# Performance work log

Hardware: AMD Instinct MI355X
Metric: run time of the kernel (lower is better)

The kernel has to match this reference:

```python
import jax, jax.numpy as jnp
import numpy as np

D = 1536          # d_model
H = 12            # n_heads // 2 for chunk attention
HD = D // H       # head dim = 128
MAXC = 256        # max_chunks
MAXLEN = 1024     # max_seq_length (size embedding table)
THRESH = 0.5      # boundary threshold (init value of the learned param)


def _gelu(v):
    return jax.nn.gelu(v, approximate=False)  # torch nn.GELU default (erf)


def _cos(a, b):
    # F.cosine_similarity with eps=1e-8
    na = jnp.maximum(jnp.linalg.norm(a, axis=-1), 1e-8)
    nb = jnp.maximum(jnp.linalg.norm(b, axis=-1), 1e-8)
    return jnp.sum(a * b, axis=-1) / (na * nb)


def _interp1d(y, L_out):
    # F.interpolate(mode='linear', align_corners=False) on [B, L_in] -> [B, L_out]
    L_in = y.shape[1]
    src = jnp.clip((jnp.arange(L_out, dtype=y.dtype) + 0.5) * (L_in / L_out) - 0.5, 0.0, L_in - 1)
    i0 = jnp.floor(src).astype(jnp.int32)
    i1 = jnp.minimum(i0 + 1, L_in - 1)
    w = src - i0.astype(y.dtype)
    return y[:, i0] * (1.0 - w) + y[:, i1] * w


def setup_inputs() -> dict:
    key = jax.random.key(0)
    ks = jax.random.split(key, 16)
    B, S = 4, 1024
    rn = lambda k, sh, s=0.02: jax.random.normal(k, sh, dtype=jnp.float32) * s
    return {
        'x': jax.random.normal(ks[0], (B, S, D), dtype=jnp.float32),
        'Wp': rn(ks[1], (D, D)), 'bp': jnp.zeros((D,), jnp.float32),
        'detW1': rn(ks[2], (3, D, 2 * D)), 'detb1': jnp.zeros((3, D), jnp.float32),
        'detW2': rn(ks[3], (3, D // 2, D)), 'detb2': jnp.zeros((3, D // 2), jnp.float32),
        'detW3': rn(ks[4], (3, D // 2)), 'detb3': jnp.zeros((3,), jnp.float32),
        'in_proj_w': rn(ks[5], (3 * D, D)), 'in_proj_b': jnp.zeros((3 * D,), jnp.float32),
        'out_w': rn(ks[6], (D, D)), 'out_b': jnp.zeros((D,), jnp.float32),
        'size_emb': jax.random.normal(ks[7], (MAXLEN, D), dtype=jnp.float32),
        'pos_enc': rn(ks[8], (1, MAXC, D)),
        'procW1': rn(ks[9], (2 * D, D)), 'procb1': jnp.zeros((2 * D,), jnp.float32),
        'procW2': rn(ks[10], (D, 2 * D)), 'procb2': jnp.zeros((D,), jnp.float32),
        'ln_g': jnp.ones((D,), jnp.float32), 'ln_b': jnp.zeros((D,), jnp.float32),
    }


def reference(x, Wp, bp, detW1, detb1, detW2, detb2, detW3, detb3,
              in_proj_w, in_proj_b, out_w, out_b, size_emb, pos_enc,
              procW1, procb1, procW2, procb2, ln_g, ln_b):
    B, S, d = x.shape
    # ---- DynamicSemanticChunker ----
    x_ling = x @ Wp.T + bp
    sims = []
    for scale in (1, 2, 4):
        xs = x_ling[:, ::scale]
        cs = _cos(xs[:, :-1], xs[:, 1:])           # [B, L-1]
        sims.append(_interp1d(cs, S - 1))           # [B, S-1]
    avg_sim = jnp.mean(jnp.stack(sims, 0), axis=0)
    base = 0.5 * (1.0 - avg_sim)
    bi = jnp.concatenate([x[:, :-1], x[:, 1:]], axis=-1)  # [B, S-1, 2d]
    h1 = _gelu(jnp.einsum('bsk,ndk->nbsd', bi, detW1) + detb1[:, None, None, :])
    h2 = _gelu(jnp.einsum('nbsd,nhd->nbsh', h1, detW2) + detb2[:, None, None, :])
    learned = jax.nn.sigmoid(jnp.einsum('nbsh,nh->nbs', h2, detW3) + detb3[:, None, None])
    avg_learned = jnp.mean(learned, axis=0)
    final = 0.6 * base + 0.4 * avg_learned
    boundaries = jnp.concatenate([jnp.ones((B, 1), x.dtype), final], axis=1)  # [B, S]
    # ---- EnhancedChunkLayer.create_chunks ----
    # contiguous ragged chunks == segments between boundary positions
    seg = jnp.cumsum((boundaries > THRESH).astype(jnp.int32), axis=1) - 1      # [B, S]
    # per-chunk MHA == full-seq attention with block-diagonal same-segment mask
    qkv = x @ in_proj_w.T + in_proj_b
    q, k, v = jnp.split(qkv, 3, axis=-1)
    q = q.reshape(B, S, H, HD)
    k = k.reshape(B, S, H, HD)
    v = v.reshape(B, S, H, HD)
    scores = jnp.einsum('bqhd,bkhd->bhqk', q, k) / np.sqrt(HD).astype(np.float32)
    same = (seg[:, None, :, None] == seg[:, None, None, :])                    # [B,1,S,S]
    scores = jnp.where(same, scores, jnp.asarray(-1e9, scores.dtype))
    attn = jax.nn.softmax(scores, axis=-1)
    ctx = jnp.einsum('bhqk,bkhd->bqhd', attn, v).reshape(B, S, d)
    attn_out = ctx @ out_w.T + out_b                                           # [B, S, d]
    # masked segment mean pooling; chunks with id >= MAXC are truncated away
    onehot = (seg[..., None] == jnp.arange(MAXC)).astype(x.dtype)              # [B,S,MAXC]
    sums = jnp.einsum('bsm,bsd->bmd', onehot, attn_out)
    counts = jnp.sum(onehot, axis=1)                                            # [B,MAXC]
    mean = sums / jnp.maximum(counts, 1.0)[..., None]
    clen = jnp.minimum(counts.astype(jnp.int32), MAXLEN - 1)
    sizes = size_emb[clen]                                                      # [B,MAXC,d]
    chunk = jnp.where(counts[..., None] > 0, mean + sizes, 0.0)                 # zero-pad empty
    # ---- pos encoding + chunk_processor (Linear->GELU->Linear->LayerNorm) ----
    chunk = chunk + pos_enc
    h = _gelu(chunk @ procW1.T + procb1)
    y = h @ procW2.T + procb2
    mu = jnp.mean(y, axis=-1, keepdims=True)
    var = jnp.var(y, axis=-1, keepdims=True)
    y = (y - mu) / jnp.sqrt(var + 1e-5) * ln_g + ln_b
    return y  # [B, MAXC, d]
```

## Files before the change

kernel.cpp:

```cpp
#include <hip/hip_runtime.h>
#include <hip/hip_bf16.h>
#include <math.h>

#define D_ 1536
#define S_ 1024
#define B_ 4
#define H_ 12
#define HD_ 128
#define MAXC_ 256

typedef __bf16 bf16x8_t __attribute__((ext_vector_type(8)));
typedef float f32x4_t __attribute__((ext_vector_type(4)));

__device__ __forceinline__ float gelu_f(float v) {
    return 0.5f * v * (1.0f + erff(v / 1.41421356237f));
}

__device__ __forceinline__ void split2(float a, __hip_bfloat16& h, __hip_bfloat16& l) {
    h = __float2bfloat16(a);
    l = __float2bfloat16(a - __bfloat162float(h));
}

__device__ __forceinline__ void xcd_swizzle(int& bx, int& by, int gx, int gy) {
    int nwg = gx * gy;
    int orig = by * gx + bx;
    int xcd = orig & 7;
    int q = nwg >> 3, r = nwg & 7;
    int wg = (xcd < r ? xcd * (q + 1) : r * (q + 1) + (xcd - r) * q) + (orig >> 3);
    bx = wg % gx;
    by = wg / gx;
}

template<int BM, int SPLITA, int SPLITB, int ACT, int OUT>
__global__ __launch_bounds__(256, 2)
void mfma3_gemm(const float* __restrict__ Af, const __hip_bfloat16* __restrict__ Ah,
                const __hip_bfloat16* __restrict__ Al,
                const float* __restrict__ Bf, const __hip_bfloat16* __restrict__ Bh,
                const __hip_bfloat16* __restrict__ Bl,
                const float* __restrict__ bias, int biasStride,
                float* __restrict__ Cf, __hip_bfloat16* __restrict__ Ch, __hip_bfloat16* __restrict__ Cl,
                const float* __restrict__ w3, float* __restrict__ lg,
                int K, int lda, int ldb, int ldc,
                long long aBound, long long azS, long long bzS, long long czS)
{
    __shared__ __align__(16) __hip_bfloat16 Ash[BM * 32], Asl[BM * 32];
    __shared__ __align__(16) __hip_bfloat16 Bsh[128 * 32], Bsl[128 * 32];
    const int z = blockIdx.z;
    int bxi = blockIdx.x, byi = blockIdx.y;
    xcd_swizzle(bxi, byi, gridDim.x, gridDim.y);
    const int bm = byi * BM, bn = bxi * 128;
    const int tid = threadIdx.x, lane = tid & 63, wave = tid >> 6;
    const int wm = (BM == 128) ? (wave >> 1) : 0;
    const int wn = (BM == 128) ? (wave & 1) : wave;
    constexpr int NF = (BM == 128) ? 4 : 2;
    constexpr int WC = NF * 16;
    const int fr = lane & 15, kg = lane >> 4;
    f32x4_t acc[4][NF] = {};
    constexpr int RSH = (BM == 128) ? 1 : 2;
    constexpr int NBA = (BM == 128) ? 2 : 1;
    const int ar = tid >> RSH, akb = tid & ((1 << RSH) - 1);
    const int br = tid >> 1, bkb = tid & 1;

    bf16x8_t rAh[NBA], rAl[NBA], rBh[2], rBl[2];
    float4 rAf[NBA][2], rBf[2][2];

    auto load_tile = [&](int k0) {
        #pragma unroll
        for (int j = 0; j < NBA; ++j) {
            int skg = akb * NBA + j;
            long long base = (long long)(bm + ar) * lda + azS * z + k0 + skg * 8;
            if (SPLITA) {
                #pragma unroll
                for (int q = 0; q < 2; ++q) {
                    float4 v = make_float4(0.f, 0.f, 0.f, 0.f);
                    if (base + q * 4 + 4 <= aBound) v = *reinterpret_cast<const float4*>(&Af[base + q * 4]);
                    rAf[j][q] = v;
                }
            } else {
                rAh[j] = *reinterpret_cast<const bf16x8_t*>(&Ah[base]);
                rAl[j] = *reinterpret_cast<const bf16x8_t*>(&Al[base]);
            }
        }
        #pragma unroll
        for (int j = 0; j < 2; ++j) {
            int skg = bkb * 2 + j;
            long long base = (long long)(bn + br) * ldb + bzS * z + k0 + skg * 8;
            if (SPLITB) {
                #pragma unroll
                for (int q = 0; q < 2; ++q)
                    rBf[j][q] = *reinterpret_cast<const float4*>(&Bf[base + q * 4]);
            } else {
                rBh[j] = *reinterpret_cast<const bf16x8_t*>(&Bh[base]);
                rBl[j] = *reinterpret_cast<const bf16x8_t*>(&Bl[base]);
            }
        }
    };

    auto write_tile = [&]() {
        #pragma unroll
        for (int j = 0; j < NBA; ++j) {
            int skg = akb * NBA + j;
            int blk = ar * 4 + (skg ^ ((ar >> 1) & 3));
            if (SPLITA) {
                float av[8];
                *reinterpret_cast<float4*>(&av[0]) = rAf[j][0];
                *reinterpret_cast<float4*>(&av[4]) = rAf[j][1];
                __hip_bfloat16 hh[8], ll[8];
                #pragma unroll
                for (int q = 0; q < 8; ++q) split2(av[q], hh[q], ll[q]);
                *reinterpret_cast<bf16x8_t*>(&Ash[blk * 8]) = *reinterpret_cast<bf16x8_t*>(hh);
                *reinterpret_cast<bf16x8_t*>(&Asl[blk * 8]) = *reinterpret_cast<bf16x8_t*>(ll);
            } else {
                *reinterpret_cast<bf16x8_t*>(&Ash[blk * 8]) = rAh[j];
                *reinterpret_cast<bf16x8_t*>(&Asl[blk * 8]) = rAl[j];
            }
        }
        #pragma unroll
        for (int j = 0; j < 2; ++j) {
            int skg = bkb * 2 + j;
            int blk = br * 4 + (skg ^ ((br >> 1) & 3));
            if (SPLITB) {
                float av[8];
                *reinterpret_cast<float4*>(&av[0]) = rBf[j][0];
                *reinterpret_cast<float4*>(&av[4]) = rBf[j][1];
                __hip_bfloat16 hh[8], ll[8];
                #pragma unroll
                for (int q = 0; q < 8; ++q) split2(av[q], hh[q], ll[q]);
                *reinterpret_cast<bf16x8_t*>(&Bsh[blk * 8]) = *reinterpret_cast<bf16x8_t*>(hh);
                *reinterpret_cast<bf16x8_t*>(&Bsl[blk * 8]) = *reinterpret_cast<bf16x8_t*>(ll);
            } else {
                *reinterpret_cast<bf16x8_t*>(&Bsh[blk * 8]) = rBh[j];
                *reinterpret_cast<bf16x8_t*>(&Bsl[blk * 8]) = rBl[j];
            }
        }
    };

    load_tile(0);
    write_tile();
    __syncthreads();

    for (int k0 = 0; k0 < K; k0 += 32) {
        const bool has_next = (k0 + 32) < K;
        if (has_next) load_tile(k0 + 32);

        bf16x8_t fah[4], fal[4], fbh[NF], fbl[NF];
        #pragma unroll
        for (int m = 0; m < 4; ++m) {
            int row = wm * 64 + m * 16 + fr;
            int blk = row * 4 + (kg ^ ((row >> 1) & 3));
            fah[m] = *reinterpret_cast<const bf16x8_t*>(&Ash[blk * 8]);
            fal[m] = *reinterpret_cast<const bf16x8_t*>(&Asl[blk * 8]);
        }
        #pragma unroll
        for (int n = 0; n < NF; ++n) {
            int row = wn * WC + n * 16 + fr;
            int blk = row * 4 + (kg ^ ((row >> 1) & 3));
            fbh[n] = *reinterpret_cast<const bf16x8_t*>(&Bsh[blk * 8]);
            fbl[n] = *reinterpret_cast<const bf16x8_t*>(&Bsl[blk * 8]);
        }
        #pragma unroll
        for (int m = 0; m < 4; ++m)
            #pragma unroll
            for (int n = 0; n < NF; ++n) {
                acc[m][n] = __builtin_amdgcn_mfma_f32_16x16x32_bf16(fah[m], fbh[n], acc[m][n], 0, 0, 0);
                acc[m][n] = __builtin_amdgcn_mfma_f32_16x16x32_bf16(fah[m], fbl[n], acc[m][n], 0, 0, 0);
                acc[m][n] = __builtin_amdgcn_mfma_f32_16x16x32_bf16(fal[m], fbh[n], acc[m][n], 0, 0, 0);
            }

        if (has_next) {
            __syncthreads();
            write_tile();
            __syncthreads();
        }
    }

    const int fq = lane >> 4;
    const float* bp_ = bias + (long long)biasStride * z;

    if constexpr (OUT == 2) {
        float psum[4][4] = {};
        #pragma unroll
        for (int n = 0; n < NF; ++n) {
            int col = bn + wn * WC + n * 16 + fr;
            float bv = bp_[col];
            float wv = w3[(long long)biasStride * z + col];
            #pragma unroll
            for (int m = 0; m < 4; ++m)
                #pragma unroll
                for (int r = 0; r < 4; ++r) {
                    float v = acc[m][n][r] + bv;
                    v = gelu_f(v);
                    psum[m][r] += v * wv;
                }
        }
        #pragma unroll
        for (int m = 0; m < 4; ++m)
            #pragma unroll
            for (int r = 0; r < 4; ++r) {
                float p = psum[m][r];
                p += __shfl_xor(p, 1);
                p += __shfl_xor(p, 2);
                p += __shfl_xor(p, 4);
                p += __shfl_xor(p, 8);
                if (fr == 0) {
                    int row = bm + wm * 64 + m * 16 + fq * 4 + r;
                    atomicAdd(&lg[czS * z + row], p);
                }
            }
        return;
    }

    #pragma unroll
    for (int n = 0; n < NF; ++n) {
        int col = bn + wn * WC + n * 16 + fr;
        float bv = bp_[col];
        #pragma unroll
        for (int m = 0; m < 4; ++m) {
            int row0 = bm + wm * 64 + m * 16 + fq * 4;
            #pragma unroll
            for (int r = 0; r < 4; ++r) {
                float v = acc[m][n][r] + bv;
                if (ACT == 1) v = gelu_f(v);
                long long ci = czS * z + (long long)(row0 + r) * ldc + col;
                if constexpr (OUT == 0) {
                    Cf[ci] = v;
                } else {
                    __hip_bfloat16 hh, ll;
                    split2(v, hh, ll);
                    Ch[ci] = hh; Cl[ci] = ll;
                }
            }
        }
    }
}

template<int ACT, int OUT_BF16>
__global__ __launch_bounds__(256)
void mfma_gemm(const __hip_bfloat16* __restrict__ A, const __hip_bfloat16* __restrict__ Bw,
               const float* __restrict__ bias, void* __restrict__ Cout,
               int M, int N, int K)
{
    __shared__ __align__(16) __hip_bfloat16 As[128 * 32];
    __shared__ __align__(16) __hip_bfloat16 Bs[128 * 32];
    const int tid = threadIdx.x;
    const int lane = tid & 63;
    const int wave = tid >> 6;
    const int wm = wave >> 1, wn = wave & 1;
    int bxi = blockIdx.x, byi = blockIdx.y;
    xcd_swizzle(bxi, byi, gridDim.x, gridDim.y);
    const int bm = byi * 128, bn = bxi * 128;
    const int srow = tid >> 2;
    const int skg = tid & 3;
    const int fr = lane & 15, kg = lane >> 4;

    f32x4_t acc[4][4] = {};
    bf16x8_t rA[2], rB[2];

    auto load_tile = [&](int k0) {
        #pragma unroll
        for (int it = 0; it < 2; ++it) {
            int r = srow + it * 64;
            rA[it] = *reinterpret_cast<const bf16x8_t*>(&A[(long long)(bm + r) * K + k0 + skg * 8]);
            rB[it] = *reinterpret_cast<const bf16x8_t*>(&Bw[(long long)(bn + r) * K + k0 + skg * 8]);
        }
    };
    auto write_tile = [&]() {
        #pragma unroll
        for (int it = 0; it < 2; ++it) {
            int r = srow + it * 64;
            int blk = r * 4 + (skg ^ ((r >> 1) & 3));
            *reinterpret_cast<bf16x8_t*>(&As[blk * 8]) = rA[it];
            *reinterpret_cast<bf16x8_t*>(&Bs[blk * 8]) = rB[it];
        }
    };

    load_tile(0);
    write_tile();
    __syncthreads();

    for (int k0 = 0; k0 < K; k0 += 32) {
        const bool has_next = (k0 + 32) < K;
        if (has_next) load_tile(k0 + 32);

        bf16x8_t af[4], bfr[4];
        #pragma unroll
        for (int m = 0; m < 4; ++m) {
            int row = wm * 64 + m * 16 + fr;
            af[m] = *reinterpret_cast<const bf16x8_t*>(&As[(row * 4 + (kg ^ ((row >> 1) & 3))) * 8]);
        }
        #pragma unroll
        for (int n = 0; n < 4; ++n) {
            int row = wn * 64 + n * 16 + fr;
            bfr[n] = *reinterpret_cast<const bf16x8_t*>(&Bs[(row * 4 + (kg ^ ((row >> 1) & 3))) * 8]);
        }
        #pragma unroll
        for (int m = 0; m < 4; ++m)
            #pragma unroll
            for (int n = 0; n < 4; ++n)
                acc[m][n] = __builtin_amdgcn_mfma_f32_16x16x32_bf16(af[m], bfr[n], acc[m][n], 0, 0, 0);

        if (has_next) {
            __syncthreads();
            write_tile();
            __syncthreads();
        }
    }
    const int fq = lane >> 4;
    #pragma unroll
    for (int n = 0; n < 4; ++n) {
        int col = bn + wn * 64 + n * 16 + fr;
        float bv = bias[col];
        #pragma unroll
        for (int m = 0; m < 4; ++m) {
            int row0 = bm + wm * 64 + m * 16 + fq * 4;
            #pragma unroll
            for (int r = 0; r < 4; ++r) {
                float v = acc[m][n][r] + bv;
                if (ACT == 1) v = gelu_f(v);
                if (OUT_BF16) ((__hip_bfloat16*)Cout)[(long long)(row0 + r) * N + col] = __float2bfloat16(v);
                else          ((float*)Cout)[(long long)(row0 + r) * N + col] = v;
            }
        }
    }
}

__global__ __launch_bounds__(256)
void f2b_kernel(const float* __restrict__ in, __hip_bfloat16* __restrict__ out, int n4)
{
    int i = blockIdx.x * 256 + threadIdx.x;
    if (i >= n4) return;
    float4 v = reinterpret_cast<const float4*>(in)[i];
    __hip_bfloat16 h[4] = { __float2bfloat16(v.x), __float2bfloat16(v.y),
                            __float2bfloat16(v.z), __float2bfloat16(v.w) };
    reinterpret_cast<short4*>(out)[i] = *reinterpret_cast<short4*>(h);
}

__global__ __launch_bounds__(256)
void split_kernel(const float* __restrict__ in, __hip_bfloat16* __restrict__ oh,
                  __hip_bfloat16* __restrict__ ol, int n4)
{
    int i = blockIdx.x * 256 + threadIdx.x;
    if (i >= n4) return;
    float4 v = reinterpret_cast<const float4*>(in)[i];
    __hip_bfloat16 h[4], l[4];
    split2(v.x, h[0], l[0]); split2(v.y, h[1], l[1]);
    split2(v.z, h[2], l[2]); split2(v.w, h[3], l[3]);
    reinterpret_cast<short4*>(oh)[i] = *reinterpret_cast<short4*>(h);
    reinterpret_cast<short4*>(ol)[i] = *reinterpret_cast<short4*>(l);
}

__global__ __launch_bounds__(64)
void cs_kernel(const float* __restrict__ xl, float* __restrict__ cs)
{
    int idx = blockIdx.x;
    int b = blockIdx.y;
    int sc, i, off;
    if (idx < 1023)      { sc = 1; i = idx;        off = 0;    }
    else if (idx < 1534) { sc = 2; i = idx - 1023; off = 1023; }
    else                 { sc = 4; i = idx - 1534; off = 1534; }
    const float* ra = xl + ((long long)b * S_ + (long long)i * sc) * D_;
    const float* rb = ra + (long long)sc * D_;
    int lane = threadIdx.x;
    float dp = 0.f, na = 0.f, nb = 0.f;
    for (int d = lane; d < D_; d += 64) {
        float a = ra[d], c = rb[d];
        dp += a * c; na += a * a; nb += c * c;
    }
    #pragma unroll
    for (int o = 32; o; o >>= 1) {
        dp += __shfl_down(dp, o);
        na += __shfl_down(na, o);
        nb += __shfl_down(nb, o);
    }
    if (lane == 0) {
        float den = fmaxf(sqrtf(na), 1e-8f) * fmaxf(sqrtf(nb), 1e-8f);
        cs[(long long)b * 1789 + off + i] = dp / den;
    }
}

__global__ void final_kernel(const float* __restrict__ cs, const float* __restrict__ logits,
                             const float* __restrict__ b3, float* __restrict__ fin)
{
    int g = blockIdx.x * blockDim.x + threadIdx.x;
    if (g >= B_ * 1023) return;
    int b = g / 1023, t = g % 1023;
    const float* c = cs + (long long)b * 1789;
    float v0 = c[t];
    const float r2 = (float)(511.0 / 1023.0);
    float src2 = fminf(fmaxf(((float)t + 0.5f) * r2 - 0.5f, 0.0f), 510.0f);
    int i0 = (int)floorf(src2);
    int i1 = min(i0 + 1, 510);
    float w2 = src2 - (float)i0;
    float v1 = c[1023 + i0] * (1.0f - w2) + c[1023 + i1] * w2;
    const float r4 = (float)(255.0 / 1023.0);
    float src4 = fminf(fmaxf(((float)t + 0.5f) * r4 - 0.5f, 0.0f), 254.0f);
    int j0 = (int)floorf(src4);
    int j1 = min(j0 + 1, 254);
    float w4 = src4 - (float)j0;
    float v2 = c[1534 + j0] * (1.0f - w4) + c[1534 + j1] * w4;
    float avg = ((v0 + v1) + v2) / 3.0f;
    float base = 0.5f * (1.0f - avg);
    int rr = b * 1024 + t;
    float l0 = 1.0f / (1.0f + expf(-(logits[0 * 4096 + rr] + b3[0])));
    float l1 = 1.0f / (1.0f + expf(-(logits[1 * 4096 + rr] + b3[1])));
    float l2 = 1.0f / (1.0f + expf(-(logits[2 * 4096 + rr] + b3[2])));
    float al = ((l0 + l1) + l2) / 3.0f;
    fin[g] = 0.6f * base + 0.4f * al;
}

__global__ __launch_bounds__(64)
void seg_kernel(const float* __restrict__ fin, int* __restrict__ seg)
{
    int b = blockIdx.x;
    int lane = threadIdx.x;
    int loc[16];
    int cnt = 0;
    #pragma unroll
    for (int i = 0; i < 16; ++i) {
        int t = lane * 16 + i;
        int v = (t >= 1 && fin[b * 1023 + t - 1] > 0.5f) ? 1 : 0;
        cnt += v;
        loc[i] = cnt;
    }
    int inc = cnt;
    #pragma unroll
    for (int o = 1; o < 64; o <<= 1) {
        int u = __shfl_up(inc, o);
        if (lane >= o) inc += u;
    }
    int ex = inc - cnt;
    #pragma unroll
    for (int i = 0; i < 16; ++i) {
        int t = lane * 16 + i;
        seg[b * S_ + t] = ex + loc[i];
    }
}

__global__ void segrange_kernel(const float* __restrict__ fin, const int* __restrict__ seg,
                                int* __restrict__ sstart, int* __restrict__ send,
                                int* __restrict__ cfirst, int* __restrict__ ccount)
{
    int gs = blockIdx.x * blockDim.x + threadIdx.x;
    if (gs >= B_ * S_) return;
    int b = gs / S_, s = gs % S_;
    const float* f = fin + b * 1023;
    int t = s;
    while (t > 0 && !(f[t - 1] > 0.5f)) --t;
    int e = s;
    while (e < 1023 && !(f[e] > 0.5f)) ++e;
    sstart[gs] = t;
    send[gs] = e + 1;
    if (s == t) {
        int m = seg[gs];
        if (m < MAXC_) { cfirst[b * MAXC_ + m] = t; ccount[b * MAXC_ + m] = e + 1 - t; }
    }
}

__global__ __launch_bounds__(64)
void attn_kernel(const __hip_bfloat16* __restrict__ qkv, const int* __restrict__ sstart,
                 const int* __restrict__ send, __hip_bfloat16* __restrict__ ctx)
{
    int gs = blockIdx.x;
    int h = blockIdx.y;
    int lane = threadIdx.x;
    int b = gs >> 10;
    const __hip_bfloat16* qrow = qkv + (long long)gs * 4608 + h * HD_;
    float q0 = __bfloat162float(qrow[lane]), q1 = __bfloat162float(qrow[lane + 64]);
    int st = sstart[gs], en = send[gs];
    float m = -INFINITY, l = 0.f, a0 = 0.f, a1 = 0.f;
    for (int t = st; t < en; ++t) {
        long long krow = ((long long)(b * S_ + t)) * 4608 + 1536 + h * HD_;
        float p = q0 * __bfloat162float(qkv[krow + lane]) + q1 * __bfloat162float(qkv[krow + lane + 64]);
        #pragma unroll
        for (int o = 32; o; o >>= 1) p += __shfl_xor(p, o);
        p = p / 11.3137084989847603904f;
        float nm = fmaxf(m, p);
        float scale = expf(m - nm);
        float w = expf(p - nm);
        long long vrow = ((long long)(b * S_ + t)) * 4608 + 3072 + h * HD_;
        l = l * scale + w;
        a0 = a0 * scale + w * __bfloat162float(qkv[vrow + lane]);
        a1 = a1 * scale + w * __bfloat162float(qkv[vrow + lane + 64]);
        m = nm;
    }
    float inv = 1.0f / l;
    ctx[(long long)gs * D_ + h * HD_ + lane] = __float2bfloat16(a0 * inv);
    ctx[(long long)gs * D_ + h * HD_ + lane + 64] = __float2bfloat16(a1 * inv);
}

__global__ __launch_bounds__(256)
void chunk_kernel(const float* __restrict__ attn_out, const int* __restrict__ cfirst,
                  const int* __restrict__ ccount, const float* __restrict__ size_emb,
                  const float* __restrict__ pos_enc, __hip_bfloat16* __restrict__ chunk)
{
    int m = blockIdx.x, b = blockIdx.y;
    int cnt = ccount[b * MAXC_ + m];
    for (int d = threadIdx.x; d < D_; d += 256) {
        float v;
        if (cnt > 0) {
            int first = cfirst[b * MAXC_ + m];
            float ssum = 0.f;
            for (int t = 0; t < cnt; ++t)
                ssum += attn_out[((long long)(b * S_ + first + t)) * D_ + d];
            float mean = ssum / (float)cnt;
            int clen = min(cnt, 1023);
            v = mean + size_emb[(long long)clen * D_ + d];
        } else {
            v = 0.f;
        }
        v += pos_enc[m * D_ + d];
        chunk[((long long)(b * MAXC_ + m)) * D_ + d] = __float2bfloat16(v);
    }
}

__global__ __launch_bounds__(256)
void ln_kernel(const float* __restrict__ y0, const float* __restrict__ g,
               const float* __restrict__ bb, float* __restrict__ out)
{
    int r = blockIdx.x;
    const float* row = y0 + (long long)r * D_;
    float loc[6];
    float s = 0.f;
    #pragma unroll
    for (int i = 0; i < 6; ++i) { loc[i] = row[threadIdx.x + i * 256]; s += loc[i]; }
    __shared__ float red[256];
    red[threadIdx.x] = s; __syncthreads();
    for (int o = 128; o; o >>= 1) { if (threadIdx.x < o) red[threadIdx.x] += red[threadIdx.x + o]; __syncthreads(); }
    float mu = red[0] / 1536.0f;
    __syncthreads();
    float s2 = 0.f;
    #pragma unroll
    for (int i = 0; i < 6; ++i) { float d = loc[i] - mu; s2 += d * d; }
    red[threadIdx.x] = s2; __syncthreads();
    for (int o = 128; o; o >>= 1) { if (threadIdx.x < o) red[threadIdx.x] += red[threadIdx.x + o]; __syncthreads(); }
    float var = red[0] / 1536.0f;
    float inv = 1.0f / sqrtf(var + 1e-5f);
    #pragma unroll
    for (int i = 0; i < 6; ++i) {
        int d = threadIdx.x + i * 256;
        out[(long long)r * D_ + d] = (loc[i] - mu) * inv * g[d] + bb[d];
    }
}

extern "C" void kernel_launch(void* const* d_in, const int* in_sizes, int n_in,
                              void* d_out, int out_size, void* d_ws, size_t ws_size,
                              hipStream_t stream)
{
    const float* x         = (const float*)d_in[0];
    const float* Wp        = (const float*)d_in[1];
    const float* bp        = (const float*)d_in[2];
    const float* detW1     = (const float*)d_in[3];
    const float* detb1     = (const float*)d_in[4];
    const float* detW2     = (const float*)d_in[5];
    const float* detb2     = (const float*)d_in[6];
    const float* detW3     = (const float*)d_in[7];
    const float* detb3     = (const float*)d_in[8];
    const float* in_proj_w = (const float*)d_in[9];
    const float* in_proj_b = (const float*)d_in[10];
    const float* out_w     = (const float*)d_in[11];
    const float* out_b     = (const float*)d_in[12];
    const float* size_emb  = (const float*)d_in[13];
    const float* pos_enc   = (const float*)d_in[14];
    const float* procW1    = (const float*)d_in[15];
    const float* procb1    = (const float*)d_in[16];
    const float* procW2    = (const float*)d_in[17];
    const float* procb2    = (const float*)d_in[18];
    const float* ln_g      = (const float*)d_in[19];
    const float* ln_b      = (const float*)d_in[20];
    float* out = (float*)d_out;

    const bool big = ws_size >= (size_t)192 * 1024 * 1024;

    char* ws = (char*)d_ws;
    float*          xlingf = (float*)(ws + 0);
    __hip_bfloat16* Wph    = (__hip_bfloat16*)(ws + 25165824);
    __hip_bfloat16* Wpl    = (__hip_bfloat16*)(ws + 29884416);
    __hip_bfloat16* h1h    = (__hip_bfloat16*)(ws + 0);
    __hip_bfloat16* h1l    = (__hip_bfloat16*)(ws + 37748736);
    __hip_bfloat16* W1h_s  = (__hip_bfloat16*)(ws + 75497472);
    __hip_bfloat16* W1l_s  = (__hip_bfloat16*)(ws + 94371840);
    __hip_bfloat16* W2h_s  = (__hip_bfloat16*)(ws + 75497472);
    __hip_bfloat16* W2l_s  = (__hip_bfloat16*)(ws + 82575360);
    __hip_bfloat16* xh     = (__hip_bfloat16*)(ws + 75497472);
    __hip_bfloat16* xl     = (__hip_bfloat16*)(ws + 88082432);
    __hip_bfloat16* W1h_b  = (__hip_bfloat16*)(ws + 125829120);
    __hip_bfloat16* W1l_b  = (__hip_bfloat16*)(ws + 154140672);
    __hip_bfloat16* W2h_b  = (__hip_bfloat16*)(ws + 125829120);
    __hip_bfloat16* W2l_b  = (__hip_bfloat16*)(ws + 132907008);
    __hip_bfloat16* xb_s       = (__hip_bfloat16*)(ws + 0);
    __hip_bfloat16* in_proj_wb = (__hip_bfloat16*)(ws + 12582912);
    __hip_bfloat16* qkvb       = (__hip_bfloat16*)(ws + 26738688);
    __hip_bfloat16* ctxb       = (__hip_bfloat16*)(ws + 64487424);
    __hip_bfloat16* out_wb     = (__hip_bfloat16*)(ws + 12582912);
    float*          attno      = (float*)(ws + 77070336);
    __hip_bfloat16* chunkb     = (__hip_bfloat16*)(ws + 0);
    __hip_bfloat16* procW1b    = (__hip_bfloat16*)(ws + 3145728);
    __hip_bfloat16* hmidb      = (__hip_bfloat16*)(ws + 12582912);
    __hip_bfloat16* procW2b    = (__hip_bfloat16*)(ws + 18874368);
    float*          y0         = (float*)(ws + 28311552);
    char* sm = ws + 113246208;
    float* csb    = (float*)(sm + 0);
    float* logits = (float*)(sm + 28672);
    float* fin    = (float*)(sm + 77824);
    int*   seg    = (int*)  (sm + 94208);
    int*   sstart = (int*)  (sm + 110592);
    int*   send   = (int*)  (sm + 126976);
    int*   cfirst = (int*)  (sm + 143360);
    int*   ccount = (int*)  (sm + 147456);

    const long long SLICE_W1 = 4718592LL;
    const long long SLICE_W2 = 1179648LL;
    const long long H1_Z     = 6291456LL;

    split_kernel<<<(2359296 / 4 + 255) / 256, 256, 0, stream>>>(Wp, Wph, Wpl, 2359296 / 4);
    if (big)
        split_kernel<<<(6291456 / 4 + 255) / 256, 256, 0, stream>>>(x, xh, xl, 6291456 / 4);

    if (big)
        mfma3_gemm<128, 0, 0, 0, 0><<<dim3(12, 32, 1), 256, 0, stream>>>(
            nullptr, xh, xl, nullptr, Wph, Wpl, bp, 0,
            xlingf, nullptr, nullptr, nullptr, nullptr,
            1536, 1536, 1536, 1536, 0LL, 0LL, 0LL, 0LL);
    else
        mfma3_gemm<64, 1, 0, 0, 0><<<dim3(12, 64, 1), 256, 0, stream>>>(
            x, nullptr, nullptr, nullptr, Wph, Wpl, bp, 0,
            xlingf, nullptr, nullptr, nullptr, nullptr,
            1536, 1536, 1536, 1536, 6291456LL, 0LL, 0LL, 0LL);
    cs_kernel<<<dim3(1789, 4), 64, 0, stream>>>(xlingf, csb);

    if (big) {
        split_kernel<<<(14155776 / 4 + 255) / 256, 256, 0, stream>>>(detW1, W1h_b, W1l_b, 14155776 / 4);
        mfma3_gemm<128, 0, 0, 1, 1><<<dim3(12, 32, 3), 256, 0, stream>>>(
            nullptr, xh, xl, nullptr, W1h_b, W1l_b, detb1, 1536,
            nullptr, h1h, h1l, nullptr, nullptr,
            3072, 1536, 3072, 1536, 0LL, 0LL, SLICE_W1, H1_Z);
    } else {
        split_kernel<<<(2 * 4718592 / 4 + 255) / 256, 256, 0, stream>>>(detW1, W1h_s, W1l_s, 2 * 4718592 / 4);
        mfma3_gemm<128, 1, 0, 1, 1><<<dim3(12, 32, 2), 256, 0, stream>>>(
            x, nullptr, nullptr, nullptr, W1h_s, W1l_s, detb1, 1536,
            nullptr, h1h, h1l, nullptr, nullptr,
            3072, 1536, 3072, 1536, 6291456LL, 0LL, SLICE_W1, H1_Z);
        split_kernel<<<(4718592 / 4 + 255) / 256, 256, 0, stream>>>(detW1 + 2 * SLICE_W1, W1h_s, W1l_s, 4718592 / 4);
        mfma3_gemm<64, 1, 0, 1, 1><<<dim3(12, 64, 1), 256, 0, stream>>>(
            x, nullptr, nullptr, nullptr, W1h_s, W1l_s, detb1 + 2 * 1536, 1536,
            nullptr, h1h + 2 * H1_Z, h1l + 2 * H1_Z, nullptr, nullptr,
            3072, 1536, 3072, 1536, 6291456LL, 0LL, 0LL, 0LL);
    }

    __hip_bfloat16* W2h = big ? W2h_b : W2h_s;
    __hip_bfloat16* W2l = big ? W2l_b : W2l_s;
    split_kernel<<<(3538944 / 4 + 255) / 256, 256, 0, stream>>>(detW2, W2h, W2l, 3538944 / 4);
    hipMemsetAsync(logits, 0, 3 * 4096 * sizeof(float), stream);
    mfma3_gemm<128, 0, 0, 1, 2><<<dim3(6, 32, 3), 256, 0, stream>>>(
        nullptr, h1h, h1l, nullptr, W2h, W2l, detb2, 768,
        nullptr, nullptr, nullptr, detW3, logits,
        1536, 1536, 1536, 768, 0LL, H1_Z, SLICE_W2, 4096LL);

    final_kernel<<<16, 256, 0, stream>>>(csb, logits, detb3, fin);
    seg_kernel<<<4, 64, 0, stream>>>(fin, seg);
    hipMemsetAsync(ccount, 0, B_ * MAXC_ * sizeof(int), stream);
    segrange_kernel<<<16, 256, 0, stream>>>(fin, seg, sstart, send, cfirst, ccount);

    const __hip_bfloat16* xbf;
    if (big) {
        xbf = xh;
    } else {
        f2b_kernel<<<(4096 * 1536 / 4 + 255) / 256, 256, 0, stream>>>(x, xb_s, 4096 * 1536 / 4);
        xbf = xb_s;
    }
    f2b_kernel<<<(4608 * 1536 / 4 + 255) / 256, 256, 0, stream>>>(in_proj_w, in_proj_wb, 4608 * 1536 / 4);
    mfma_gemm<0, 1><<<dim3(36, 32), 256, 0, stream>>>(xbf, in_proj_wb, in_proj_b, qkvb, 4096, 4608, 1536);

    attn_kernel<<<dim3(4096, 12), 64, 0, stream>>>(qkvb, sstart, send, ctxb);

    f2b_kernel<<<(1536 * 1536 / 4 + 255) / 256, 256, 0, stream>>>(out_w, out_wb, 1536 * 1536 / 4);
    mfma_gemm<0, 0><<<dim3(12, 32), 256, 0, stream>>>(ctxb, out_wb, out_b, attno, 4096, 1536, 1536);

    chunk_kernel<<<dim3(256, 4), 256, 0, stream>>>(attno, cfirst, ccount, size_emb, pos_enc, chunkb);

    f2b_kernel<<<(3072 * 1536 / 4 + 255) / 256, 256, 0, stream>>>(procW1, procW1b, 3072 * 1536 / 4);
    mfma_gemm<1, 1><<<dim3(24, 8), 256, 0, stream>>>(chunkb, procW1b, procb1, hmidb, 1024, 3072, 1536);
    f2b_kernel<<<(1536 * 3072 / 4 + 255) / 256, 256, 0, stream>>>(procW2, procW2b, 1536 * 3072 / 4);
    mfma_gemm<0, 0><<<dim3(12, 8), 256, 0, stream>>>(hmidb, procW2b, procb2, y0, 1024, 1536, 3072);

    ln_kernel<<<1024, 256, 0, stream>>>(y0, ln_g, ln_b, out);
}
```

Baseline: 1.110 ms.

## Double-buffer LDS in GEMM kernels and add 256-row tile kernel for detector layer-1

Converts the shared-memory tiles of the split-bf16 GEMM and the plain bf16 GEMM into ping-pong buffers, so the next tile is written while the current one is read and one barrier per K step is dropped. Adds a dedicated 256x128-tile kernel for the large-workspace detector first layer (GELU, hi/lo bf16 output), halving B-tile reloads per output. The extra LDS and the larger accumulator array (32 fragments) raise LDS and register pressure, which may reduce occupancy below the declared two blocks per CU.

```diff
diff --git a/kernel.cpp b/kernel.cpp
--- a/kernel.cpp
+++ b/kernel.cpp
@@ -29,6 +29,126 @@
     int wg = (xcd < r ? xcd * (q + 1) : r * (q + 1) + (xcd - r) * q) + (orig >> 3);
     bx = wg % gx;
     by = wg / gx;
+}
+
+__global__ __launch_bounds__(256, 2)
+void mfma3_256(const __hip_bfloat16* __restrict__ Ah, const __hip_bfloat16* __restrict__ Al,
+               const __hip_bfloat16* __restrict__ Bh, const __hip_bfloat16* __restrict__ Bl,
+               const float* __restrict__ bias, int biasStride,
+               __hip_bfloat16* __restrict__ Ch, __hip_bfloat16* __restrict__ Cl,
+               int K, int lda, int ldb, int ldc,
+               long long azS, long long bzS, long long czS)
+{
+    __shared__ __align__(16) __hip_bfloat16 Ash[256 * 32], Asl[256 * 32];
+    __shared__ __align__(16) __hip_bfloat16 Bsh[128 * 32], Bsl[128 * 32];
+    const int z = blockIdx.z;
+    int bxi = blockIdx.x, byi = blockIdx.y;
+    xcd_swizzle(bxi, byi, gridDim.x, gridDim.y);
+    const int bm = byi * 256, bn = bxi * 128;
+    const int tid = threadIdx.x, lane = tid & 63, wave = tid >> 6;
+    const int wm = wave >> 1, wn = wave & 1;
+    const int fr = lane & 15, kg = lane >> 4;
+    f32x4_t acc[8][4] = {};
+
+    bf16x8_t rAh[4], rAl[4], rBh[2], rBl[2];
+
+    auto load_tile = [&](int k0) {
+        long long abase = (long long)(bm + tid) * lda + azS * z + k0;
+        #pragma unroll
+        for (int j = 0; j < 4; ++j) {
+            rAh[j] = *reinterpret_cast<const bf16x8_t*>(&Ah[abase + j * 8]);
+            rAl[j] = *reinterpret_cast<const bf16x8_t*>(&Al[abase + j * 8]);
+        }
+        long long bbase = (long long)(bn + (tid >> 1)) * ldb + bzS * z + k0 + (tid & 1) * 16;
+        #pragma unroll
+        for (int j = 0; j < 2; ++j) {
+            rBh[j] = *reinterpret_cast<const bf16x8_t*>(&Bh[bbase + j * 8]);
+            rBl[j] = *reinterpret_cast<const bf16x8_t*>(&Bl[bbase + j * 8]);
+        }
+    };
+    auto write_tile = [&]() {
+        int arow = tid;
+        #pragma unroll
+        for (int j = 0; j < 4; ++j) {
+            int blk = arow * 4 + (j ^ ((arow >> 1) & 3));
+            *reinterpret_cast<bf16x8_t*>(&Ash[blk * 8]) = rAh[j];
+            *reinterpret_cast<bf16x8_t*>(&Asl[blk * 8]) = rAl[j];
+        }
+        int brow = tid >> 1;
+        #pragma unroll
+        for (int j = 0; j < 2; ++j) {
+            int chunk = (tid & 1) * 2 + j;
+            int blk = brow * 4 + (chunk ^ ((brow >> 1) & 3));
+            *reinterpret_cast<bf16x8_t*>(&Bsh[blk * 8]) = rBh[j];
+            *reinterpret_cast<bf16x8_t*>(&Bsl[blk * 8]) = rBl[j];
+        }
+    };
+
+    load_tile(0);
+    write_tile();
+    __syncthreads();
+
+    for (int k0 = 0; k0 < K; k0 += 32) {
+        const bool has_next = (k0 + 32) < K;
+        if (has_next) load_tile(k0 + 32);
+
+        bf16x8_t fbh[4], fbl[4];
+        #pragma unroll
+        for (int n = 0; n < 4; ++n) {
+            int row = wn * 64 + n * 16 + fr;
+            int blk = row * 4 + (kg ^ ((row >> 1) & 3));
+            fbh[n] = *reinterpret_cast<const bf16x8_t*>(&Bsh[blk * 8]);
+            fbl[n] = *reinterpret_cast<const bf16x8_t*>(&Bsl[blk * 8]);
+        }
+        #pragma unroll
+        for (int mh = 0; mh < 2; ++mh) {
+            bf16x8_t fah[4], fal[4];
+            #pragma unroll
+            for (int m = 0; m < 4; ++m) {
+                int row = wm * 128 + mh * 64 + m * 16 + fr;
+                int blk = row * 4 + (kg ^ ((row >> 1) & 3));
+                fah[m] = *reinterpret_cast<const bf16x8_t*>(&Ash[blk * 8]);
+                fal[m] = *reinterpret_cast<const bf16x8_t*>(&Asl[blk * 8]);
+            }
+            #pragma unroll
+            for (int m = 0; m < 4; ++m)
+                #pragma unroll
+                for (int n = 0; n < 4; ++n) {
+                    acc[mh * 4 + m][n] = __builtin_amdgcn_mfma_f32_16x16x32_bf16(fah[m], fbh[n], acc[mh * 4 + m][n], 0, 0, 0);
+                    acc[mh * 4 + m][n] = __builtin_amdgcn_mfma_f32_16x16x32_bf16(fah[m], fbl[n], acc[mh * 4 + m][n], 0, 0, 0);
+                    acc[mh * 4 + m][n] = __builtin_amdgcn_mfma_f32_16x16x32_bf16(fal[m], fbh[n], acc[mh * 4 + m][n], 0, 0, 0);
+                }
+        }
+
+        if (has_next) {
+            __syncthreads();
+            write_tile();
+            __syncthreads();
+        }
+    }
+
+    const int fq = lane >> 4;
+    const float* bp_ = bias + (long long)biasStride * z;
+    #pragma unroll
+    for (int n = 0; n < 4; ++n) {
+        int col = bn + wn * 64 + n * 16 + fr;
+        float bv = bp_[col];
+        #pragma unroll
+        for (int mh = 0; mh < 2; ++mh)
+            #pragma unroll
+            for (int m = 0; m < 4; ++m) {
+                int row0 = bm + wm * 128 + mh * 64 + m * 16 + fq * 4;
+                #pragma unroll
+                for (int r = 0; r < 4; ++r) {
+                    float v = acc[mh * 4 + m][n][r] + bv;
+                    v = gelu_f(v);
+                    long long ci = czS * z + (long long)(row0 + r) * ldc + col;
+                    __hip_bfloat16 hh, ll;
+                    split2(v, hh, ll);
+                    Ch[ci] = hh; Cl[ci] = ll;
+                }
+            }
+    }
 }
 
 template<int BM, int SPLITA, int SPLITB, int ACT, int OUT>
@@ -43,8 +163,8 @@
                 int K, int lda, int ldb, int ldc,
                 long long aBound, long long azS, long long bzS, long long czS)
 {
-    __shared__ __align__(16) __hip_bfloat16 Ash[BM * 32], Asl[BM * 32];
-    __shared__ __align__(16) __hip_bfloat16 Bsh[128 * 32], Bsl[128 * 32];
+    __shared__ __align__(16) __hip_bfloat16 Ash[2][BM * 32], Asl[2][BM * 32];
+    __shared__ __align__(16) __hip_bfloat16 Bsh[2][128 * 32], Bsl[2][128 * 32];
     const int z = blockIdx.z;
     int bxi = blockIdx.x, byi = blockIdx.y;
     xcd_swizzle(bxi, byi, gridDim.x, gridDim.y);
@@ -96,7 +216,7 @@
         }
     };
 
-    auto write_tile = [&]() {
+    auto write_tile = [&](int buf) {
         #pragma unroll
         for (int j = 0; j < NBA; ++j) {
             int skg = akb * NBA + j;
@@ -108,11 +228,11 @@
                 __hip_bfloat16 hh[8], ll[8];
                 #pragma unroll
                 for (int q = 0; q < 8; ++q) split2(av[q], hh[q], ll[q]);
-                *reinterpret_cast<bf16x8_t*>(&Ash[blk * 8]) = *reinterpret_cast<bf16x8_t*>(hh);
-                *reinterpret_cast<bf16x8_t*>(&Asl[blk * 8]) = *reinterpret_cast<bf16x8_t*>(ll);
+                *reinterpret_cast<bf16x8_t*>(&Ash[buf][blk * 8]) = *reinterpret_cast<bf16x8_t*>(hh);
+                *reinterpret_cast<bf16x8_t*>(&Asl[buf][blk * 8]) = *reinterpret_cast<bf16x8_t*>(ll);
             } else {
-                *reinterpret_cast<bf16x8_t*>(&Ash[blk * 8]) = rAh[j];
-                *reinterpret_cast<bf16x8_t*>(&Asl[blk * 8]) = rAl[j];
+                *reinterpret_cast<bf16x8_t*>(&Ash[buf][blk * 8]) = rAh[j];
+                *reinterpret_cast<bf16x8_t*>(&Asl[buf][blk * 8]) = rAl[j];
             }
         }
         #pragma unroll
@@ -126,18 +246,19 @@
                 __hip_bfloat16 hh[8], ll[8];
                 #pragma unroll
                 for (int q = 0; q < 8; ++q) split2(av[q], hh[q], ll[q]);
-                *reinterpret_cast<bf16x8_t*>(&Bsh[blk * 8]) = *reinterpret_cast<bf16x8_t*>(hh);
-                *reinterpret_cast<bf16x8_t*>(&Bsl[blk * 8]) = *reinterpret_cast<bf16x8_t*>(ll);
+                *reinterpret_cast<bf16x8_t*>(&Bsh[buf][blk * 8]) = *reinterpret_cast<bf16x8_t*>(hh);
+                *reinterpret_cast<bf16x8_t*>(&Bsl[buf][blk * 8]) = *reinterpret_cast<bf16x8_t*>(ll);
             } else {
-                *reinterpret_cast<bf16x8_t*>(&Bsh[blk * 8]) = rBh[j];
-                *reinterpret_cast<bf16x8_t*>(&Bsl[blk * 8]) = rBl[j];
+                *reinterpret_cast<bf16x8_t*>(&Bsh[buf][blk * 8]) = rBh[j];
+                *reinterpret_cast<bf16x8_t*>(&Bsl[buf][blk * 8]) = rBl[j];
             }
         }
     };
 
     load_tile(0);
-    write_tile();
+    write_tile(0);
     __syncthreads();
+    int cur = 0;
 
     for (int k0 = 0; k0 < K; k0 += 32) {
         const bool has_next = (k0 + 32) < K;
@@ -148,15 +269,15 @@
         for (int m = 0; m < 4; ++m) {
             int row = wm * 64 + m * 16 + fr;
             int blk = row * 4 + (kg ^ ((row >> 1) & 3));
-            fah[m] = *reinterpret_cast<const bf16x8_t*>(&Ash[blk * 8]);
-            fal[m] = *reinterpret_cast<const bf16x8_t*>(&Asl[blk * 8]);
+            fah[m] = *reinterpret_cast<const bf16x8_t*>(&Ash[cur][blk * 8]);
+            fal[m] = *reinterpret_cast<const bf16x8_t*>(&Asl[cur][blk * 8]);
         }
         #pragma unroll
         for (int n = 0; n < NF; ++n) {
             int row = wn * WC + n * 16 + fr;
             int blk = row * 4 + (kg ^ ((row >> 1) & 3));
-            fbh[n] = *reinterpret_cast<const bf16x8_t*>(&Bsh[blk * 8]);
-            fbl[n] = *reinterpret_cast<const bf16x8_t*>(&Bsl[blk * 8]);
+            fbh[n] = *reinterpret_cast<const bf16x8_t*>(&Bsh[cur][blk * 8]);
+            fbl[n] = *reinterpret_cast<const bf16x8_t*>(&Bsl[cur][blk * 8]);
         }
         #pragma unroll
         for (int m = 0; m < 4; ++m)
@@ -168,9 +289,9 @@
             }
 
         if (has_next) {
+            write_tile(cur ^ 1);
             __syncthreads();
-            write_tile();
-            __syncthreads();
+            cur ^= 1;
         }
     }
 
@@ -240,8 +361,8 @@
                const float* __restrict__ bias, void* __restrict__ Cout,
                int M, int N, int K)
 {
-    __shared__ __align__(16) __hip_bfloat16 As[128 * 32];
-    __shared__ __align__(16) __hip_bfloat16 Bs[128 * 32];
+    __shared__ __align__(16) __hip_bfloat16 As[2][128 * 32];
+    __shared__ __align__(16) __hip_bfloat16 Bs[2][128 * 32];
     const int tid = threadIdx.x;
     const int lane = tid & 63;
     const int wave = tid >> 6;
@@ -264,19 +385,20 @@
             rB[it] = *reinterpret_cast<const bf16x8_t*>(&Bw[(long long)(bn + r) * K + k0 + skg * 8]);
         }
     };
-    auto write_tile = [&]() {
+    auto write_tile = [&](int buf) {
         #pragma unroll
         for (int it = 0; it < 2; ++it) {
             int r = srow + it * 64;
             int blk = r * 4 + (skg ^ ((r >> 1) & 3));
-            *reinterpret_cast<bf16x8_t*>(&As[blk * 8]) = rA[it];
-            *reinterpret_cast<bf16x8_t*>(&Bs[blk * 8]) = rB[it];
+            *reinterpret_cast<bf16x8_t*>(&As[buf][blk * 8]) = rA[it];
+            *reinterpret_cast<bf16x8_t*>(&Bs[buf][blk * 8]) = rB[it];
         }
     };
 
     load_tile(0);
-    write_tile();
+    write_tile(0);
     __syncthreads();
+    int cur = 0;
 
     for (int k0 = 0; k0 < K; k0 += 32) {
         const bool has_next = (k0 + 32) < K;
@@ -286,12 +408,12 @@
         #pragma unroll
         for (int m = 0; m < 4; ++m) {
             int row = wm * 64 + m * 16 + fr;
-            af[m] = *reinterpret_cast<const bf16x8_t*>(&As[(row * 4 + (kg ^ ((row >> 1) & 3))) * 8]);
+            af[m] = *reinterpret_cast<const bf16x8_t*>(&As[cur][(row * 4 + (kg ^ ((row >> 1) & 3))) * 8]);
         }
         #pragma unroll
         for (int n = 0; n < 4; ++n) {
             int row = wn * 64 + n * 16 + fr;
-            bfr[n] = *reinterpret_cast<const bf16x8_t*>(&Bs[(row * 4 + (kg ^ ((row >> 1) & 3))) * 8]);
+            bfr[n] = *reinterpret_cast<const bf16x8_t*>(&Bs[cur][(row * 4 + (kg ^ ((row >> 1) & 3))) * 8]);
         }
         #pragma unroll
         for (int m = 0; m < 4; ++m)
@@ -300,9 +422,9 @@
                 acc[m][n] = __builtin_amdgcn_mfma_f32_16x16x32_bf16(af[m], bfr[n], acc[m][n], 0, 0, 0);
 
         if (has_next) {
+            write_tile(cur ^ 1);
             __syncthreads();
-            write_tile();
-            __syncthreads();
+            cur ^= 1;
         }
     }
     const int fq = lane >> 4;
@@ -630,10 +752,10 @@
 
     if (big) {
         split_kernel<<<(14155776 / 4 + 255) / 256, 256, 0, stream>>>(detW1, W1h_b, W1l_b, 14155776 / 4);
-        mfma3_gemm<128, 0, 0, 1, 1><<<dim3(12, 32, 3), 256, 0, stream>>>(
-            nullptr, xh, xl, nullptr, W1h_b, W1l_b, detb1, 1536,
-            nullptr, h1h, h1l, nullptr, nullptr,
-            3072, 1536, 3072, 1536, 0LL, 0LL, SLICE_W1, H1_Z);
+        mfma3_256<<<dim3(12, 16, 3), 256, 0, stream>>>(
+            xh, xl, W1h_b, W1l_b, detb1, 1536,
+            h1h, h1l, 3072, 1536, 3072, 1536,
+            0LL, SLICE_W1, H1_Z);
     } else {
         split_kernel<<<(2 * 4718592 / 4 + 255) / 256, 256, 0, stream>>>(detW1, W1h_s, W1l_s, 2 * 4718592 / 4);
         mfma3_gemm<128, 1, 0, 1, 1><<<dim3(12, 32, 2), 256, 0, stream>>>(
```

New measurement: 1.332 ms. 1.2x slower.
